# Kernel tuning notes

Measured on AMD Instinct MI355X. Metric: run time of the kernel, lower is better.

## Reference

```python
import jax, jax.numpy as jnp
import numpy as np

CHEB_K = 3
HIDDEN = 64
HORIZON = 12
OUT_DIM = 1


def _supports(E, K):
    # adaptive adjacency: softmax(relu(E E^T)) rows, Chebyshev polynomial stack [K, N, N]
    A = jax.nn.softmax(jax.nn.relu(E @ E.T), axis=1)
    N = E.shape[0]
    s = [jnp.eye(N, dtype=E.dtype), A]
    for _ in range(2, K):
        s.append(2.0 * (A @ s[-1]) - s[-2])
    return jnp.stack(s, axis=0)


def _gconv(x, supports, W, b):
    # x: [B,N,C], supports: [K,N,N], W: [N,K,C,O], b: [N,O] -> [B,N,O]
    xg = jnp.einsum('knm,bmc->bnkc', supports, x)
    return jnp.einsum('bnkc,nkco->bno', xg, W) + b


def _agcrn_layer(x_seq, supports, gW, gb, uW, ub):
    # x_seq: [B,T,N,C]; returns full hidden sequence [B,T,N,H]
    B, T, N, _ = x_seq.shape
    h0 = jnp.zeros((B, N, HIDDEN), dtype=x_seq.dtype)

    def step(h, x):
        zr = jax.nn.sigmoid(_gconv(jnp.concatenate([x, h], axis=-1), supports, gW, gb))
        z, r = zr[..., :HIDDEN], zr[..., HIDDEN:]
        hc = jnp.tanh(_gconv(jnp.concatenate([x, z * h], axis=-1), supports, uW, ub))
        h_new = r * h + (1.0 - r) * hc
        return h_new, h_new

    _, hs = jax.lax.scan(step, h0, jnp.swapaxes(x_seq, 0, 1))  # [T,B,N,H]
    return jnp.swapaxes(hs, 0, 1)


def _forward(source, E, pools, conv_w, conv_b):
    supports = _supports(E, CHEB_K)
    cur = source
    for (gwp, gbp, uwp, ubp) in pools:
        # per-node weights from embedding pool (hoisted: E is constant over time)
        gW = jnp.einsum('nd,dkio->nkio', E, gwp)
        gb = E @ gbp
        uW = jnp.einsum('nd,dkio->nkio', E, uwp)
        ub = E @ ubp
        cur = _agcrn_layer(cur, supports, gW, gb, uW, ub)
    last = cur[:, -1]  # [B,N,H]
    # end_conv: Conv2d(1, horizon*out_dim, kernel=(1,H)) == linear over H per node
    y = jnp.einsum('bnh,oh->bon', last, conv_w) + conv_b[None, :, None]  # [B, horizon*out, N]
    B, _, N = y.shape
    y = y.reshape(B, HORIZON, OUT_DIM, N).transpose(0, 1, 3, 2)  # [B, horizon, N, out_dim]
    return y


def setup_inputs() -> dict:
    key = jax.random.key(0)
    ks = jax.random.split(key, 12)
    B, T, N, C, D, H = 64, 12, 2000, 1, 16, HIDDEN
    s = 0.1  # keep gates/tanh unsaturated
    return {
        'source': jax.random.normal(ks[0], (B, T, N, C), jnp.float32),
        'node_embeddings': jax.random.normal(ks[1], (N, D), jnp.float32),
        'gate_wpool_0': jax.random.normal(ks[2], (D, CHEB_K, C + H, 2 * H), jnp.float32) * s,
        'gate_bpool_0': jax.random.normal(ks[3], (D, 2 * H), jnp.float32) * s,
        'update_wpool_0': jax.random.normal(ks[4], (D, CHEB_K, C + H, H), jnp.float32) * s,
        'update_bpool_0': jax.random.normal(ks[5], (D, H), jnp.float32) * s,
        'gate_wpool_1': jax.random.normal(ks[6], (D, CHEB_K, 2 * H, 2 * H), jnp.float32) * s,
        'gate_bpool_1': jax.random.normal(ks[7], (D, 2 * H), jnp.float32) * s,
        'update_wpool_1': jax.random.normal(ks[8], (D, CHEB_K, 2 * H, H), jnp.float32) * s,
        'update_bpool_1': jax.random.normal(ks[9], (D, H), jnp.float32) * s,
        'conv_w': jax.random.normal(ks[10], (HORIZON * OUT_DIM, H), jnp.float32) * s,
        'conv_b': jax.random.normal(ks[11], (HORIZON * OUT_DIM,), jnp.float32) * s,
    }


def reference(source, node_embeddings, gate_wpool_0, gate_bpool_0, update_wpool_0,
              update_bpool_0, gate_wpool_1, gate_bpool_1, update_wpool_1,
              update_bpool_1, conv_w, conv_b):
    pools = [
        (gate_wpool_0, gate_bpool_0, update_wpool_0, update_bpool_0),
        (gate_wpool_1, gate_bpool_1, update_wpool_1, update_bpool_1),
    ]
    return _forward(source, node_embeddings, pools, conv_w, conv_b)
```

## Files before the change

### kernel.cpp

```cpp
#include <hip/hip_runtime.h>
#include <hip/hip_bf16.h>
#include <math.h>

#define NN 2000
#define DD 16
#define BB 64
#define TT 12
#define HH 64
#define MR 4000
#define SCL 2048.0f
#define ISCL (1.0f / 2048.0f)

typedef _Float16 f16;
typedef __attribute__((ext_vector_type(8))) _Float16 frag8h;
typedef __attribute__((ext_vector_type(4))) float floatx4;

__device__ inline float fin(float v) {
  return (v == v && v > -1e30f && v < 1e30f) ? v : 0.f;
}
__device__ inline float sigmoid_safe(float x) {
  float e = expf(-fabsf(x));
  float s = 1.f / (1.f + e);
  return x >= 0.f ? s : 1.f - s;
}
__device__ inline float tanh_safe(float x) {
  float e = expf(-2.f * fabsf(x));
  float r = (1.f - e) / (1.f + e);
  return x >= 0.f ? r : -r;
}
__device__ inline void split16(float v, f16& hi, f16& lo) {
  hi = (f16)v;
  lo = (f16)((v - (float)hi) * SCL);
}
__device__ inline void gll16(const void* g, void* l) {
  __builtin_amdgcn_global_load_lds((const __attribute__((address_space(1))) void*)g,
                                   (__attribute__((address_space(3))) void*)l, 16, 0, 0);
}

__global__ void kzero(float* p, int n) {
  int i = blockIdx.x * 256 + threadIdx.x;
  if (i < n) p[i] = 0.f;
}

__global__ __launch_bounds__(256) void ka(const float* __restrict__ E,
                                          float* __restrict__ A) {
  __shared__ float s[NN];
  __shared__ float red[256];
  int n = blockIdx.x;
  float en[DD];
#pragma unroll
  for (int d = 0; d < DD; ++d) en[d] = fin(E[n * DD + d]);
  float lmax = 0.f;
  for (int m = threadIdx.x; m < NN; m += 256) {
    float acc = 0.f;
#pragma unroll
    for (int d = 0; d < DD; ++d) acc += en[d] * fin(E[m * DD + d]);
    acc = fmaxf(acc, 0.f);
    s[m] = acc;
    lmax = fmaxf(lmax, acc);
  }
  red[threadIdx.x] = lmax;
  __syncthreads();
  for (int w = 128; w > 0; w >>= 1) {
    if (threadIdx.x < w) red[threadIdx.x] = fmaxf(red[threadIdx.x], red[threadIdx.x + w]);
    __syncthreads();
  }
  float mx = red[0];
  __syncthreads();
  float lsum = 0.f;
  for (int m = threadIdx.x; m < NN; m += 256) {
    float e = expf(s[m] - mx);
    s[m] = e;
    lsum += e;
  }
  red[threadIdx.x] = lsum;
  __syncthreads();
  for (int w = 128; w > 0; w >>= 1) {
    if (threadIdx.x < w) red[threadIdx.x] += red[threadIdx.x + w];
    __syncthreads();
  }
  float inv = 1.f / red[0];
  for (int m = threadIdx.x; m < NN; m += 256) A[(size_t)n * NN + m] = s[m] * inv;
}

#define TM 64
#define TK 32
__global__ __launch_bounds__(256) void kg(const float* __restrict__ A,
                                          const float* __restrict__ V,
                                          float* __restrict__ C, int cols) {
  __shared__ float As[TK][TM + 1];
  __shared__ float Bs[TK][TM + 1];
  int r0 = blockIdx.x * TM;
  int c0 = blockIdx.y * TM;
  int tid = threadIdx.x;
  int tx = tid % 16;
  int ty = tid / 16;
  float acc[4][4];
#pragma unroll
  for (int i = 0; i < 4; ++i)
#pragma unroll
    for (int j = 0; j < 4; ++j) acc[i][j] = 0.f;
  for (int k0 = 0; k0 < NN; k0 += TK) {
    for (int i = tid; i < TM * TK; i += 256) {
      int rr = i / TK, kk = i % TK;
      int gr = r0 + rr, gk = k0 + kk;
      As[kk][rr] = (gr < NN && gk < NN) ? A[(size_t)gr * NN + gk] : 0.f;
    }
    for (int i = tid; i < TK * TM; i += 256) {
      int kk = i / TM, cc = i % TM;
      int gk = k0 + kk, gc = c0 + cc;
      Bs[kk][cc] = (gk < NN && gc < cols) ? V[(size_t)gk * cols + gc] : 0.f;
    }
    __syncthreads();
#pragma unroll 4
    for (int kk = 0; kk < TK; ++kk) {
      float a[4], b[4];
#pragma unroll
      for (int i = 0; i < 4; ++i) a[i] = As[kk][ty * 4 + i];
#pragma unroll
      for (int j = 0; j < 4; ++j) b[j] = Bs[kk][tx * 4 + j];
#pragma unroll
      for (int i = 0; i < 4; ++i)
#pragma unroll
        for (int j = 0; j < 4; ++j) acc[i][j] += a[i] * b[j];
    }
    __syncthreads();
  }
#pragma unroll
  for (int i = 0; i < 4; ++i) {
    int gr = r0 + ty * 4 + i;
    if (gr >= NN) continue;
#pragma unroll
    for (int j = 0; j < 4; ++j) {
      int gc = c0 + tx * 4 + j;
      if (gc < cols) C[(size_t)gr * cols + gc] = acc[i][j];
    }
  }
}

__global__ void ksplitM(const float* __restrict__ A, const float* __restrict__ A2,
                        f16* __restrict__ Mh, f16* __restrict__ Ml) {
  int i = blockIdx.x * 256 + threadIdx.x;
  if (i >= MR * NN) return;
  int m = i / NN;
  int k = i % NN;
  float v;
  if (m < NN) v = A[(size_t)m * NN + k];
  else {
    int mm = m - NN;
    v = 2.f * A2[(size_t)mm * NN + k] - (mm == k ? 1.f : 0.f);
  }
  f16 hi, lo;
  split16(v, hi, lo);
  Mh[i] = hi;
  Ml[i] = lo;
}

__global__ __launch_bounds__(256) void kconvT(const float* __restrict__ V,
                                              f16* __restrict__ Th,
                                              f16* __restrict__ Tl, int cols) {
  __shared__ float sh[32][33];
  int k0 = blockIdx.x * 32;
  int c0 = blockIdx.y * 32;
  int tx = threadIdx.x % 32;
  int ty = threadIdx.x / 32;
#pragma unroll
  for (int i = 0; i < 4; ++i) {
    int r = k0 + ty + i * 8;
    int c = c0 + tx;
    sh[ty + i * 8][tx] = (r < NN && c < cols) ? V[(size_t)r * cols + c] : 0.f;
  }
  __syncthreads();
#pragma unroll
  for (int i = 0; i < 4; ++i) {
    int cc = c0 + ty + i * 8;
    int kk = k0 + tx;
    if (cc < cols && kk < NN) {
      f16 hi, lo;
      split16(sh[tx][ty + i * 8], hi, lo);
      Th[(size_t)cc * NN + kk] = hi;
      Tl[(size_t)cc * NN + kk] = lo;
    }
  }
}

#define KT 32
__global__ __launch_bounds__(256, 2) void kmm(const f16* __restrict__ Mh,
                                              const f16* __restrict__ Ml,
                                              const f16* __restrict__ Bh,
                                              const f16* __restrict__ Bl,
                                              float* __restrict__ C1,
                                              float* __restrict__ C2, int cols) {
  __shared__ __align__(16) f16 Ash[128 * KT];
  __shared__ __align__(16) f16 Asl[128 * KT];
  __shared__ __align__(16) f16 Bsh[128 * KT];
  __shared__ __align__(16) f16 Bsl[128 * KT];
  int tid = threadIdx.x;
  int lane = tid & 63;
  int wave = tid >> 6;
  int wr = wave >> 1;
  int wc = wave & 1;
  int gx = gridDim.x;
  int nwg = gx * gridDim.y;
  int wg = blockIdx.y * gx + blockIdx.x;
  int q = nwg >> 3, r = nwg & 7;
  int xcd = wg & 7, lid = wg >> 3;
  int swz = (xcd < r ? xcd * (q + 1) : r * (q + 1) + (xcd - r) * q) + lid;
  int bx = swz % gx;
  int by = swz / gx;
  floatx4 acc0[4][4], acc1[4][4];
#pragma unroll
  for (int i = 0; i < 4; ++i)
#pragma unroll
    for (int j = 0; j < 4; ++j) {
      acc0[i][j] = (floatx4){0.f, 0.f, 0.f, 0.f};
      acc1[i][j] = (floatx4){0.f, 0.f, 0.f, 0.f};
    }
  const frag8h zf = {0, 0, 0, 0, 0, 0, 0, 0};

  auto comp = [&]() {
    frag8h ah[4], al[4], bh[4], bl[4];
#pragma unroll
    for (int mi = 0; mi < 4; ++mi) {
      int jr = wr * 4 + mi;
      ah[mi] = *(const frag8h*)(&Ash[jr * 512 + lane * 8]);
      al[mi] = *(const frag8h*)(&Asl[jr * 512 + lane * 8]);
    }
#pragma unroll
    for (int ni = 0; ni < 4; ++ni) {
      int jc = wc * 4 + ni;
      bh[ni] = *(const frag8h*)(&Bsh[jc * 512 + lane * 8]);
      bl[ni] = *(const frag8h*)(&Bsl[jc * 512 + lane * 8]);
    }
#pragma unroll
    for (int mi = 0; mi < 4; ++mi)
#pragma unroll
      for (int ni = 0; ni < 4; ++ni) {
        acc0[mi][ni] = __builtin_amdgcn_mfma_f32_16x16x32_f16(ah[mi], bh[ni], acc0[mi][ni], 0, 0, 0);
        acc1[mi][ni] = __builtin_amdgcn_mfma_f32_16x16x32_f16(ah[mi], bl[ni], acc1[mi][ni], 0, 0, 0);
        acc1[mi][ni] = __builtin_amdgcn_mfma_f32_16x16x32_f16(al[mi], bh[ni], acc1[mi][ni], 0, 0, 0);
      }
  };

  const int lr = lane & 15;
  const int lq = lane >> 4;
  for (int k0 = 0; k0 + KT <= NN; k0 += KT) {
#pragma unroll
    for (int jj = 0; jj < 2; ++jj) {
      int j = wave * 2 + jj;
      int r2 = j * 16 + lr;
      size_t ko = (size_t)k0 + lq * 8;
      int gra = bx * 128 + r2;
      if (gra < MR) {
        gll16(Mh + (size_t)gra * NN + ko, Ash + j * 512);
        gll16(Ml + (size_t)gra * NN + ko, Asl + j * 512);
      }
      int grb = by * 128 + r2;
      if (grb < cols) {
        gll16(Bh + (size_t)grb * NN + ko, Bsh + j * 512);
        gll16(Bl + (size_t)grb * NN + ko, Bsl + j * 512);
      }
    }
    __syncthreads();
    comp();
    __syncthreads();
  }
  {
    int k0 = (NN / KT) * KT;
    if (k0 < NN) {
      for (int c = tid; c < 512; c += 256) {
        int j = c >> 6;
        int ll = c & 63;
        int qq = ll >> 4;
        int rr = ll & 15;
        int r2 = j * 16 + rr;
        int gk = k0 + qq * 8;
        bool kok = (gk + 8 <= NN);
        int gra = bx * 128 + r2;
        bool aok = kok && (gra < MR);
        size_t ga = (size_t)gra * NN + gk;
        *(frag8h*)(&Ash[c * 8]) = aok ? *(const frag8h*)(Mh + ga) : zf;
        *(frag8h*)(&Asl[c * 8]) = aok ? *(const frag8h*)(Ml + ga) : zf;
        int grb = by * 128 + r2;
        bool bok = kok && (grb < cols);
        size_t gb = (size_t)grb * NN + gk;
        *(frag8h*)(&Bsh[c * 8]) = bok ? *(const frag8h*)(Bh + gb) : zf;
        *(frag8h*)(&Bsl[c * 8]) = bok ? *(const frag8h*)(Bl + gb) : zf;
      }
      __syncthreads();
      comp();
      __syncthreads();
    }
  }
#pragma unroll
  for (int mi = 0; mi < 4; ++mi) {
#pragma unroll
    for (int ni = 0; ni < 4; ++ni) {
#pragma unroll
      for (int reg = 0; reg < 4; ++reg) {
        int row = bx * 128 + wr * 64 + mi * 16 + (lane >> 4) * 4 + reg;
        int col = by * 128 + wc * 64 + ni * 16 + (lane & 15);
        if (col >= cols || row >= MR) continue;
        float v = acc0[mi][ni][reg] + acc1[mi][ni][reg] * ISCL;
        if (row < NN) C1[(size_t)row * cols + col] = v;
        else C2[(size_t)(row - NN) * cols + col] = v;
      }
    }
  }
}

__global__ void kx(const float* __restrict__ src, float* __restrict__ xb,
                   int t, int b0, int CB) {
  int i = blockIdx.x * 256 + threadIdx.x;
  if (i >= NN * CB) return;
  int bb = i % CB;
  int n = i / CB;
  xb[i] = fin(src[((size_t)(b0 + bb) * TT + t) * NN + n]);
}

__global__ void kxa(const float* __restrict__ src, float* __restrict__ xa,
                    int b0, int CB) {
  int i = blockIdx.x * 256 + threadIdx.x;
  if (i >= NN * TT * CB) return;
  int bb = i % CB;
  int t = (i / CB) % TT;
  int n = i / (CB * TT);
  xa[i] = fin(src[((size_t)(b0 + bb) * TT + t) * NN + n]);
}

__global__ void kmulz(float* __restrict__ zb, const float* __restrict__ h, int n) {
  int i = blockIdx.x * 256 + threadIdx.x;
  if (i < n) zb[i] = zb[i] * h[i];
}

template <int O, int CB>
__global__ __launch_bounds__(256) void kgc(
    const float* __restrict__ x0, const float* __restrict__ x1, const float* __restrict__ x2,
    const float* __restrict__ wp, int Ctot, int base_c, int nC, int ldn,
    const float* __restrict__ E, const float* __restrict__ bp,
    int act, int accum, float* outA, float* outB,
    int update, const float* __restrict__ rb, float* hio) {
  __shared__ float xs[8][CB + 1];
  __shared__ float ws[8][O];
  __shared__ float esm[DD];
  int n = blockIdx.x;
  int tid = threadIdx.x;
  int to = tid % 16;
  int tb = tid / 16;
  if (tid < DD) esm[tid] = fin(E[n * DD + tid]);
  __syncthreads();
  constexpr int NO = O / 16;
  constexpr int NB = CB / 16;
  float acc[NB][NO];
#pragma unroll
  for (int i = 0; i < NB; ++i)
#pragma unroll
    for (int j = 0; j < NO; ++j) acc[i][j] = 0.f;
  const size_t nb = (size_t)n * CB;
  const size_t nx = (size_t)n * ldn;
  for (int k = 0; k < 3; ++k) {
    const float* xk = (k == 0) ? x0 : (k == 1) ? x1 : x2;
    for (int c0 = 0; c0 < nC; c0 += 8) {
      int chunk = (nC - c0 < 8) ? (nC - c0) : 8;
      for (int i = tid; i < chunk * CB; i += 256) {
        int cc = i % chunk;
        int b = i / chunk;
        xs[cc][b] = xk[nx + (size_t)b * nC + c0 + cc];
      }
      for (int i = tid; i < chunk * O; i += 256) {
        int o = i % O;
        int cc = i / O;
        int crow = base_c + c0 + cc;
        float wa = 0.f;
#pragma unroll
        for (int d = 0; d < DD; ++d)
          wa += esm[d] * fin(wp[((size_t)(d * 3 + k) * Ctot + crow) * O + o]);
        ws[cc][o] = wa;
      }
      __syncthreads();
      for (int cc = 0; cc < chunk; ++cc) {
        float xv[NB];
#pragma unroll
        for (int i = 0; i < NB; ++i) xv[i] = xs[cc][tb + 16 * i];
#pragma unroll
        for (int j = 0; j < NO; ++j) {
          float wv = ws[cc][to + 16 * j];
#pragma unroll
          for (int i = 0; i < NB; ++i) acc[i][j] += xv[i] * wv;
        }
      }
      __syncthreads();
    }
  }
#pragma unroll
  for (int i2 = 0; i2 < NB; ++i2) {
    int b = tb + 16 * i2;
#pragma unroll
    for (int j = 0; j < NO; ++j) {
      int o = to + 16 * j;
      float r = acc[i2][j];
      float* dst = (o < HH || !outB) ? (outA + (nb + b) * HH + (o % HH))
                                     : (outB + (nb + b) * HH + (o - HH));
      if (accum) r += *dst;
      if (bp) {
        float ba = 0.f;
#pragma unroll
        for (int d = 0; d < DD; ++d) ba += esm[d] * fin(bp[d * O + o]);
        r += ba;
      }
      r = fin(r);
      if (act == 1) r = sigmoid_safe(r);
      else if (act == 2) r = tanh_safe(r);
      if (update) {
        float rg = rb[(nb + b) * HH + o];
        float hold = hio[(nb + b) * HH + o];
        hio[(nb + b) * HH + o] = rg * hold + (1.f - rg) * r;
      } else {
        *dst = r;
      }
    }
  }
}

__global__ void kfin(const float* __restrict__ h1, const float* __restrict__ cw,
                     const float* __restrict__ cb, float* __restrict__ out,
                     int b0, int CB) {
  int idx = blockIdx.x * 256 + threadIdx.x;
  if (idx >= CB * TT * NN) return;
  int n = idx % NN;
  int o = (idx / NN) % TT;
  int bb = idx / (NN * TT);
  const float* hp = h1 + ((size_t)n * CB + bb) * HH;
  float acc = fin(cb[o]);
#pragma unroll
  for (int hh = 0; hh < HH; ++hh) acc += hp[hh] * fin(cw[o * HH + hh]);
  out[((size_t)(b0 + bb) * TT + o) * NN + n] = fin(acc);
}

template <int CB>
static void run_chunks(const float* src, const float* E,
                       const float* gwp0, const float* gbp0,
                       const float* uwp0, const float* ubp0,
                       const float* gwp1, const float* gbp1,
                       const float* uwp1, const float* ubp1,
                       const float* cw, const float* cb,
                       float* out, f16* Mh, f16* Ml,
                       char* wsp, size_t off0, bool roomy, hipStream_t stream) {
  size_t off = off0;
  auto allocf = [&](size_t nelem) {
    float* p = (float*)(wsp + off);
    off += (nelem * 4 + 255) & ~(size_t)255;
    return p;
  };
  auto alloch = [&](size_t nelem) {
    f16* p = (f16*)(wsp + off);
    off += (nelem * 2 + 255) & ~(size_t)255;
    return p;
  };
  const int C = CB * HH;
  const int XC = TT * CB;
  const size_t NC = (size_t)NN * C;
  float* P1  = allocf(NC);
  float* P2  = allocf(NC);
  float* h0  = allocf(NC);
  float* h1  = allocf(NC);
  float* zb  = allocf(NC);
  float* rbf = allocf(NC);
  float* hc  = allocf(NC);
  f16* vh = alloch(NC);
  f16* vl = alloch(NC);
  float *P1c = nullptr, *P2c = nullptr;
  float *xa = nullptr, *xb1a = nullptr, *xb2a = nullptr;
  float *xb0 = nullptr, *xb1 = nullptr, *xb2 = nullptr;
  f16 *xth, *xtl;
  if (roomy) {
    P1c = allocf(NC);
    P2c = allocf(NC);
    xa   = allocf((size_t)NN * XC);
    xb1a = allocf((size_t)NN * XC);
    xb2a = allocf((size_t)NN * XC);
    xth = alloch((size_t)NN * XC);
    xtl = alloch((size_t)NN * XC);
  } else {
    xb0 = allocf((size_t)NN * CB);
    xb1 = allocf((size_t)NN * CB);
    xb2 = allocf((size_t)NN * CB);
    xth = alloch((size_t)NN * CB);
    xtl = alloch((size_t)NN * CB);
  }

  const int EW = (int)((NC + 255) / 256);
  const dim3 gConv((NN + 31) / 32, (C + 31) / 32);
  const dim3 gMM((MR + 127) / 128, (C + 127) / 128);
  float* nul = nullptr;

  auto chain_to = [&](const float* V, float* D1, float* D2) {
    kconvT<<<gConv, 256, 0, stream>>>(V, vh, vl, C);
    kmm<<<gMM, 256, 0, stream>>>(Mh, Ml, vh, vl, D1, D2, C);
  };

  for (int b0 = 0; b0 < BB; b0 += CB) {
    kzero<<<EW, 256, 0, stream>>>(h0, (int)NC);
    kzero<<<EW, 256, 0, stream>>>(h1, (int)NC);
    if (roomy) {
      kxa<<<((NN * XC) + 255) / 256, 256, 0, stream>>>(src, xa, b0, CB);
      dim3 gcx((NN + 31) / 32, (XC + 31) / 32);
      kconvT<<<gcx, 256, 0, stream>>>(xa, xth, xtl, XC);
      dim3 gmx((MR + 127) / 128, (XC + 127) / 128);
      kmm<<<gmx, 256, 0, stream>>>(Mh, Ml, xth, xtl, xb1a, xb2a, XC);
    }
    for (int t = 0; t < TT; ++t) {
      const bool tz = (t == 0);
      const float *xt0, *xt1, *xt2;
      int xln;
      if (roomy) {
        xt0 = xa + t * CB;
        xt1 = xb1a + t * CB;
        xt2 = xb2a + t * CB;
        xln = XC;
      } else {
        kx<<<(NN * CB + 255) / 256, 256, 0, stream>>>(src, xb0, t, b0, CB);
        dim3 gcx((NN + 31) / 32, (CB + 31) / 32);
        kconvT<<<gcx, 256, 0, stream>>>(xb0, xth, xtl, CB);
        dim3 gmx((MR + 127) / 128, (CB + 127) / 128);
        kmm<<<gmx, 256, 0, stream>>>(Mh, Ml, xth, xtl, xb1, xb2, CB);
        xt0 = xb0; xt1 = xb1; xt2 = xb2;
        xln = CB;
      }
      const float *g1, *g2;
      if (tz) { g1 = h0; g2 = h0; }
      else if (roomy) { g1 = P1c; g2 = P2c; }
      else { chain_to(h0, P1, P2); g1 = P1; g2 = P2; }
      kgc<128, CB><<<NN, 256, 0, stream>>>(h0, g1, g2, gwp0, 65, 1, 64, C, E, nullptr,
                                           0, 0, zb, rbf, 0, nul, nul);
      kgc<128, CB><<<NN, 256, 0, stream>>>(xt0, xt1, xt2, gwp0, 65, 0, 1, xln, E, gbp0,
                                           1, 1, zb, rbf, 0, nul, nul);
      kgc<64, CB><<<NN, 256, 0, stream>>>(xt0, xt1, xt2, uwp0, 65, 0, 1, xln, E, nullptr,
                                          0, 0, hc, nul, 0, nul, nul);
      kmulz<<<EW, 256, 0, stream>>>(zb, h0, (int)NC);
      if (tz) {
        kgc<64, CB><<<NN, 256, 0, stream>>>(zb, zb, zb, uwp0, 65, 1, 64, C, E, ubp0,
                                            2, 1, hc, nul, 1, rbf, h0);
      } else {
        chain_to(zb, P1, P2);
        kgc<64, CB><<<NN, 256, 0, stream>>>(zb, P1, P2, uwp0, 65, 1, 64, C, E, ubp0,
                                            2, 1, hc, nul, 1, rbf, h0);
      }
      if (tz) {
        kgc<128, CB><<<NN, 256, 0, stream>>>(h1, h1, h1, gwp1, 128, 64, 64, C, E, nullptr,
                                             0, 0, zb, rbf, 0, nul, nul);
      } else {
        chain_to(h1, P1, P2);
        kgc<128, CB><<<NN, 256, 0, stream>>>(h1, P1, P2, gwp1, 128, 64, 64, C, E, nullptr,
                                             0, 0, zb, rbf, 0, nul, nul);
      }
      float* q1 = roomy ? P1c : P1;
      float* q2 = roomy ? P2c : P2;
      chain_to(h0, q1, q2);
      kgc<128, CB><<<NN, 256, 0, stream>>>(h0, q1, q2, gwp1, 128, 0, 64, C, E, gbp1,
                                           1, 1, zb, rbf, 0, nul, nul);
      kgc<64, CB><<<NN, 256, 0, stream>>>(h0, q1, q2, uwp1, 128, 0, 64, C, E, nullptr,
                                          0, 0, hc, nul, 0, nul, nul);
      kmulz<<<EW, 256, 0, stream>>>(zb, h1, (int)NC);
      if (tz) {
        kgc<64, CB><<<NN, 256, 0, stream>>>(zb, zb, zb, uwp1, 128, 64, 64, C, E, ubp1,
                                            2, 1, hc, nul, 1, rbf, h1);
      } else {
        chain_to(zb, P1, P2);
        kgc<64, CB><<<NN, 256, 0, stream>>>(zb, P1, P2, uwp1, 128, 64, 64, C, E, ubp1,
                                            2, 1, hc, nul, 1, rbf, h1);
      }
    }
    kfin<<<(CB * TT * NN + 255) / 256, 256, 0, stream>>>(h1, cw, cb, out, b0, CB);
  }
}

extern "C" void kernel_launch(void* const* d_in, const int* in_sizes, int n_in,
                              void* d_out, int out_size, void* d_ws, size_t ws_size,
                              hipStream_t stream) {
  const float* src  = (const float*)d_in[0];
  const float* E    = (const float*)d_in[1];
  const float* gwp0 = (const float*)d_in[2];
  const float* gbp0 = (const float*)d_in[3];
  const float* uwp0 = (const float*)d_in[4];
  const float* ubp0 = (const float*)d_in[5];
  const float* gwp1 = (const float*)d_in[6];
  const float* gbp1 = (const float*)d_in[7];
  const float* uwp1 = (const float*)d_in[8];
  const float* ubp1 = (const float*)d_in[9];
  const float* cw   = (const float*)d_in[10];
  const float* cb   = (const float*)d_in[11];
  float* out = (float*)d_out;
  (void)in_sizes; (void)n_in; (void)out_size;

  char* wsp = (char*)d_ws;
  size_t off = 0;
  f16* Mh = (f16*)(wsp + off); off += ((size_t)MR * NN * 2 + 255) & ~(size_t)255;
  f16* Ml = (f16*)(wsp + off); off += ((size_t)MR * NN * 2 + 255) & ~(size_t)255;
  size_t off0 = off;
  float* A  = (float*)(wsp + off0);
  float* A2 = (float*)(wsp + off0 + (((size_t)NN * NN * 4 + 255) & ~(size_t)255));

  ka<<<NN, 256, 0, stream>>>(E, A);
  {
    dim3 g((NN + TM - 1) / TM, (NN + TM - 1) / TM);
    kg<<<g, 256, 0, stream>>>(A, A, A2, NN);
  }
  ksplitM<<<(MR * NN + 255) / 256, 256, 0, stream>>>(A, A2, Mh, Ml);

  if (ws_size >= (size_t)400 * 1000 * 1000) {
    run_chunks<64>(src, E, gwp0, gbp0, uwp0, ubp0, gwp1, gbp1, uwp1, ubp1,
                   cw, cb, out, Mh, Ml, wsp, off0, true, stream);
  } else if (ws_size >= (size_t)320 * 1000 * 1000) {
    run_chunks<64>(src, E, gwp0, gbp0, uwp0, ubp0, gwp1, gbp1, uwp1, ubp1,
                   cw, cb, out, Mh, Ml, wsp, off0, false, stream);
  } else if (ws_size >= (size_t)225 * 1000 * 1000) {
    run_chunks<32>(src, E, gwp0, gbp0, uwp0, ubp0, gwp1, gbp1, uwp1, ubp1,
                   cw, cb, out, Mh, Ml, wsp, off0, true, stream);
  } else if (ws_size >= (size_t)185 * 1000 * 1000) {
    run_chunks<32>(src, E, gwp0, gbp0, uwp0, ubp0, gwp1, gbp1, uwp1, ubp1,
                   cw, cb, out, Mh, Ml, wsp, off0, false, stream);
  } else if (ws_size >= (size_t)130 * 1000 * 1000) {
    run_chunks<16>(src, E, gwp0, gbp0, uwp0, ubp0, gwp1, gbp1, uwp1, ubp1,
                   cw, cb, out, Mh, Ml, wsp, off0, true, stream);
  } else {
    run_chunks<16>(src, E, gwp0, gbp0, uwp0, ubp0, gwp1, gbp1, uwp1, ubp1,
                   cw, cb, out, Mh, Ml, wsp, off0, false, stream);
  }
}
```

Baseline: 54.50 ms.

## Double-buffer LDS tiles in split-fp16 GEMM to overlap loads with MFMA

Doubles the shared-memory A/B hi/lo tile buffers so the next K-slice's global-to-LDS loads are issued before computing on the current slice. Explicit vmcnt waits and raw barriers replace __syncthreads, and out-of-range rows are clamped rather than skipped so the per-stage load count stays fixed. This is meant to hide global load latency behind the MFMA work. In exchange it doubles LDS use to 64KB per block, which may lower occupancy below the 2 blocks per CU the launch bounds request, and it relies on a hand-counted vmcnt.

Result: no change. 54.58 ms (+0.1%).

```diff
diff --git a/kernel.cpp b/kernel.cpp
--- a/kernel.cpp
+++ b/kernel.cpp
@@ -191,10 +191,10 @@
                                               const f16* __restrict__ Bl,
                                               float* __restrict__ C1,
                                               float* __restrict__ C2, int cols) {
-  __shared__ __align__(16) f16 Ash[128 * KT];
-  __shared__ __align__(16) f16 Asl[128 * KT];
-  __shared__ __align__(16) f16 Bsh[128 * KT];
-  __shared__ __align__(16) f16 Bsl[128 * KT];
+  __shared__ __align__(16) f16 Ash[2][128 * KT];
+  __shared__ __align__(16) f16 Asl[2][128 * KT];
+  __shared__ __align__(16) f16 Bsh[2][128 * KT];
+  __shared__ __align__(16) f16 Bsl[2][128 * KT];
   int tid = threadIdx.x;
   int lane = tid & 63;
   int wave = tid >> 6;
@@ -218,19 +218,19 @@
     }
   const frag8h zf = {0, 0, 0, 0, 0, 0, 0, 0};
 
-  auto comp = [&]() {
+  auto comp = [&](int buf) {
     frag8h ah[4], al[4], bh[4], bl[4];
 #pragma unroll
     for (int mi = 0; mi < 4; ++mi) {
       int jr = wr * 4 + mi;
-      ah[mi] = *(const frag8h*)(&Ash[jr * 512 + lane * 8]);
-      al[mi] = *(const frag8h*)(&Asl[jr * 512 + lane * 8]);
+      ah[mi] = *(const frag8h*)(&Ash[buf][jr * 512 + lane * 8]);
+      al[mi] = *(const frag8h*)(&Asl[buf][jr * 512 + lane * 8]);
     }
 #pragma unroll
     for (int ni = 0; ni < 4; ++ni) {
       int jc = wc * 4 + ni;
-      bh[ni] = *(const frag8h*)(&Bsh[jc * 512 + lane * 8]);
-      bl[ni] = *(const frag8h*)(&Bsl[jc * 512 + lane * 8]);
+      bh[ni] = *(const frag8h*)(&Bsh[buf][jc * 512 + lane * 8]);
+      bl[ni] = *(const frag8h*)(&Bsl[buf][jc * 512 + lane * 8]);
     }
 #pragma unroll
     for (int mi = 0; mi < 4; ++mi)
@@ -244,29 +244,44 @@
 
   const int lr = lane & 15;
   const int lq = lane >> 4;
-  for (int k0 = 0; k0 + KT <= NN; k0 += KT) {
+  auto stage = [&](int buf, int k0) {
 #pragma unroll
     for (int jj = 0; jj < 2; ++jj) {
       int j = wave * 2 + jj;
       int r2 = j * 16 + lr;
       size_t ko = (size_t)k0 + lq * 8;
       int gra = bx * 128 + r2;
-      if (gra < MR) {
-        gll16(Mh + (size_t)gra * NN + ko, Ash + j * 512);
-        gll16(Ml + (size_t)gra * NN + ko, Asl + j * 512);
-      }
+      if (gra >= MR) gra = MR - 1;
+      gll16(Mh + (size_t)gra * NN + ko, &Ash[buf][j * 512]);
+      gll16(Ml + (size_t)gra * NN + ko, &Asl[buf][j * 512]);
       int grb = by * 128 + r2;
-      if (grb < cols) {
-        gll16(Bh + (size_t)grb * NN + ko, Bsh + j * 512);
-        gll16(Bl + (size_t)grb * NN + ko, Bsl + j * 512);
-      }
-    }
-    __syncthreads();
-    comp();
-    __syncthreads();
+      if (grb >= cols) grb = cols - 1;
+      gll16(Bh + (size_t)grb * NN + ko, &Bsh[buf][j * 512]);
+      gll16(Bl + (size_t)grb * NN + ko, &Bsl[buf][j * 512]);
+    }
+  };
+
+  const int NK = NN / KT;
+  stage(0, 0);
+  int cur = 0;
+  for (int ks = 0; ks < NK; ++ks) {
+    if (ks + 1 < NK) {
+      stage(cur ^ 1, (ks + 1) * KT);
+      asm volatile("s_waitcnt vmcnt(8)" ::: "memory");
+    } else {
+      asm volatile("s_waitcnt vmcnt(0)" ::: "memory");
+    }
+    __builtin_amdgcn_s_barrier();
+    asm volatile("" ::: "memory");
+    __builtin_amdgcn_sched_barrier(0);
+    comp(cur);
+    __builtin_amdgcn_sched_barrier(0);
+    asm volatile("" ::: "memory");
+    __builtin_amdgcn_s_barrier();
+    cur ^= 1;
   }
   {
-    int k0 = (NN / KT) * KT;
+    int k0 = NK * KT;
     if (k0 < NN) {
       for (int c = tid; c < 512; c += 256) {
         int j = c >> 6;
@@ -279,16 +294,16 @@
         int gra = bx * 128 + r2;
         bool aok = kok && (gra < MR);
         size_t ga = (size_t)gra * NN + gk;
-        *(frag8h*)(&Ash[c * 8]) = aok ? *(const frag8h*)(Mh + ga) : zf;
-        *(frag8h*)(&Asl[c * 8]) = aok ? *(const frag8h*)(Ml + ga) : zf;
+        *(frag8h*)(&Ash[cur][c * 8]) = aok ? *(const frag8h*)(Mh + ga) : zf;
+        *(frag8h*)(&Asl[cur][c * 8]) = aok ? *(const frag8h*)(Ml + ga) : zf;
         int grb = by * 128 + r2;
         bool bok = kok && (grb < cols);
         size_t gb = (size_t)grb * NN + gk;
-        *(frag8h*)(&Bsh[c * 8]) = bok ? *(const frag8h*)(Bh + gb) : zf;
-        *(frag8h*)(&Bsl[c * 8]) = bok ? *(const frag8h*)(Bl + gb) : zf;
+        *(frag8h*)(&Bsh[cur][c * 8]) = bok ? *(const frag8h*)(Bh + gb) : zf;
+        *(frag8h*)(&Bsl[cur][c * 8]) = bok ? *(const frag8h*)(Bl + gb) : zf;
       }
       __syncthreads();
-      comp();
+      comp(cur);
       __syncthreads();
     }
   }
```
